# Kernel optimization log

Measured on AMD Instinct MI355X. Metric: run time of the kernel, lower is better.

The kernel has to match this reference:

```python
import jax, jax.numpy as jnp
import numpy as np

MODEL_DIM = 1024
NUM_HEADS = 16
DIM_PER_HEAD = MODEL_DIM // NUM_HEADS
LN_EPS = 1e-5


def setup_inputs() -> dict:
    key = jax.random.key(0)
    ks = jax.random.split(key, 5)
    B, S, D = 2, 2048, MODEL_DIM
    scale = 1.0 / np.sqrt(D)
    x = jax.random.normal(ks[0], (B, S, D), dtype=jnp.float32)
    # nn.Linear(bias=False) weights stored as [out, in]; we apply x @ W.T
    w_q = jax.random.normal(ks[1], (D, D), dtype=jnp.float32) * scale
    w_k = jax.random.normal(ks[2], (D, D), dtype=jnp.float32) * scale
    w_v = jax.random.normal(ks[3], (D, D), dtype=jnp.float32) * scale
    w_o = jax.random.normal(ks[4], (D, D), dtype=jnp.float32) * scale
    ln_gamma = jnp.ones((D,), dtype=jnp.float32)
    ln_beta = jnp.zeros((D,), dtype=jnp.float32)
    return {"x": x, "w_q": w_q, "w_k": w_k, "w_v": w_v, "w_o": w_o,
            "ln_gamma": ln_gamma, "ln_beta": ln_beta}


def _layer_norm(x, gamma, beta):
    mu = jnp.mean(x, axis=-1, keepdims=True)
    var = jnp.var(x, axis=-1, keepdims=True)
    return (x - mu) * jax.lax.rsqrt(var + LN_EPS) * gamma + beta


def reference(x, w_q, w_k, w_v, w_o, ln_gamma, ln_beta):
    B, S, D = x.shape
    H, Dh = NUM_HEADS, DIM_PER_HEAD
    residual = x
    # projections (Linear bias=False): x @ W.T
    q = (x @ w_q.T).reshape(B, S, H, Dh).transpose(0, 2, 1, 3)  # [B,H,S,Dh]
    k = (x @ w_k.T).reshape(B, S, H, Dh).transpose(0, 2, 1, 3)
    v = (x @ w_v.T).reshape(B, S, H, Dh).transpose(0, 2, 1, 3)
    scale = Dh ** (-0.5)
    scores = jnp.einsum('bhqd,bhkd->bhqk', q, k) * scale  # [B,H,Sq,Sk]
    # FAITHFUL quirk: nn.Softmax(dim=2) normalizes over the QUERY axis (axis=2)
    attn = jax.nn.softmax(scores, axis=2)
    # dropout is identity in eval mode
    ctx = jnp.einsum('bhqk,bhkd->bhqd', attn, v)  # [B,H,S,Dh]
    ctx = ctx.transpose(0, 2, 1, 3).reshape(B, S, D)
    out = ctx @ w_o.T
    return _layer_norm(residual + out, ln_gamma, ln_beta)
```

## Files before the change

### kernel.cpp

```cpp
#include <hip/hip_runtime.h>
#include <hip/hip_bf16.h>

constexpr int kB   = 2;
constexpr int kS   = 2048;
constexpr int kD   = 1024;
constexpr int kH   = 16;
constexpr int kDh  = 64;
constexpr int kBS  = kB * kS;

typedef __attribute__((ext_vector_type(8))) short short8;
typedef __attribute__((ext_vector_type(4))) float floatx4;
typedef __attribute__((ext_vector_type(16))) float floatx16;

__device__ inline unsigned short f2b(float f) {
    __hip_bfloat16 h = __float2bfloat16(f);
    return *reinterpret_cast<unsigned short*>(&h);
}

__device__ inline float b2f(unsigned short u) {
    union { unsigned u; float f; } cv;
    cv.u = (unsigned)u << 16;
    return cv.f;
}

__device__ inline floatx4 mfma16(short8 a, short8 b, floatx4 c) {
    return __builtin_amdgcn_mfma_f32_16x16x32_bf16(a, b, c, 0, 0, 0);
}

__device__ inline floatx16 mfma32(short8 a, short8 b, floatx16 c) {
    return __builtin_amdgcn_mfma_f32_32x32x16_bf16(a, b, c, 0, 0, 0);
}

__device__ inline unsigned packbf(float a, float b) {
    union { float f; unsigned u; } x, y;
    x.f = a; y.f = b;
    return (x.u >> 16) | (y.u & 0xffff0000u);
}

__device__ inline void gload16(const unsigned short* g, unsigned short* l) {
    __builtin_amdgcn_global_load_lds(
        (const __attribute__((address_space(1))) void*)g,
        (__attribute__((address_space(3))) void*)l, 16, 0, 0);
}

__global__ void convert_kernel(const float* __restrict__ x,
                               const float* __restrict__ wq, const float* __restrict__ wk,
                               const float* __restrict__ wv, const float* __restrict__ wo,
                               unsigned short* __restrict__ xb, unsigned short* __restrict__ wb) {
#pragma unroll
    for (int it = 0; it < 4; it++) {
        int gid = blockIdx.x * blockDim.x + threadIdx.x + it * (2048 * 256);
        long i4 = (long)gid * 4;
        const float* src;
        unsigned short* dst;
        long off;
        if (i4 < (long)kBS * kD) {
            src = x; dst = xb; off = i4;
        } else {
            long w = i4 - (long)kBS * kD;
            int sel = (int)(w >> 20);
            off = w & 1048575;
            src = (sel == 0) ? wq : (sel == 1) ? wk : (sel == 2) ? wv : wo;
            dst = wb + (long)sel * 1048576;
        }
        float4 v = *(const float4*)(src + off);
        ushort4 o;
        o.x = f2b(v.x); o.y = f2b(v.y); o.z = f2b(v.z); o.w = f2b(v.w);
        *(ushort4*)(dst + off) = o;
    }
}

template <int MODE>
__launch_bounds__(256, 3)
__global__ void gemm_nt(const unsigned short* __restrict__ A,
                        const unsigned short* __restrict__ Bw,
                        void* __restrict__ Cout,
                        const float* __restrict__ resid,
                        int M, int N, int K) {
    __shared__ __align__(16) unsigned short As[128 * 64];
    __shared__ __align__(16) unsigned short Bs[128 * 64];

    const int z  = blockIdx.z;
    const unsigned short* Bp = Bw + (size_t)z * N * K;
    const int m0 = blockIdx.y * 128, n0 = blockIdx.x * 128;
    const int tid  = threadIdx.x;
    const int lane = tid & 63, wv = tid >> 6;
    const int wm = wv >> 1, wn = wv & 1;
    const int quad = lane >> 4, l16 = lane & 15;

    floatx4 acc[4][4] = {};

    const int r0 = lane >> 3;
    const int jc = ((lane & 7) ^ r0) * 8;
    const unsigned short* Ag[4];
    const unsigned short* Bg[4];
    unsigned short* Asd[4];
    unsigned short* Bsd[4];
#pragma unroll
    for (int seg = 0; seg < 4; seg++) {
        const int row = seg * 32 + wv * 8 + r0;
        Ag[seg] = A  + (size_t)(m0 + row) * K + jc;
        Bg[seg] = Bp + (size_t)(n0 + row) * K + jc;
        Asd[seg] = As + (seg * 32 + wv * 8) * 64;
        Bsd[seg] = Bs + (seg * 32 + wv * 8) * 64;
    }

    const int pk0 = (quad ^ (l16 & 7)) * 8;
    const int pk1 = ((4 + quad) ^ (l16 & 7)) * 8;

    for (int k0 = 0; k0 < K; k0 += 64) {
        __syncthreads();
#pragma unroll
        for (int seg = 0; seg < 4; seg++) {
            gload16(Ag[seg] + k0, Asd[seg]);
            gload16(Bg[seg] + k0, Bsd[seg]);
        }
        __syncthreads();

#pragma unroll
        for (int h = 0; h < 2; h++) {
            const int pk = h ? pk1 : pk0;
            short8 af[4], bf[4];
#pragma unroll
            for (int i = 0; i < 4; i++)
                af[i] = *(const short8*)(As + (wm * 64 + i * 16 + l16) * 64 + pk);
#pragma unroll
            for (int j = 0; j < 4; j++)
                bf[j] = *(const short8*)(Bs + (wn * 64 + j * 16 + l16) * 64 + pk);
#pragma unroll
            for (int i = 0; i < 4; i++)
#pragma unroll
                for (int j = 0; j < 4; j++)
                    acc[i][j] = mfma16(af[i], bf[j], acc[i][j]);
        }
    }

#pragma unroll
    for (int i = 0; i < 4; i++)
#pragma unroll
        for (int j = 0; j < 4; j++) {
            const int row = m0 + wm * 64 + i * 16 + quad * 4;
            const int col = n0 + wn * 64 + j * 16 + l16;
#pragma unroll
            for (int r = 0; r < 4; r++) {
                float v = acc[i][j][r];
                if (MODE == 0) {
                    if (z == 0) v *= 0.18033688f;
                    ((unsigned short*)Cout)[(size_t)z * M * N + (size_t)(row + r) * N + col] = f2b(v);
                } else {
                    size_t idx = (size_t)(row + r) * N + col;
                    ((float*)Cout)[idx] = v + resid[idx];
                }
            }
        }
}

__launch_bounds__(256, 3)
__global__ void gemm_nt1(const unsigned short* __restrict__ A,
                         const unsigned short* __restrict__ Bw,
                         float* __restrict__ Cout,
                         const float* __restrict__ resid,
                         int M, int N, int K) {
    __shared__ __align__(16) unsigned short As[64 * 64];
    __shared__ __align__(16) unsigned short Bs[128 * 64];

    const int m0 = blockIdx.y * 64, n0 = blockIdx.x * 128;
    const int tid  = threadIdx.x;
    const int lane = tid & 63, wv = tid >> 6;
    const int wm = wv >> 1, wn = wv & 1;
    const int quad = lane >> 4, l16 = lane & 15;

    floatx4 acc[2][4] = {};

    const int r0 = lane >> 3;
    const int jc = ((lane & 7) ^ r0) * 8;
    const unsigned short* Ag[2];
    const unsigned short* Bg[4];
    unsigned short* Asd[2];
    unsigned short* Bsd[4];
#pragma unroll
    for (int seg = 0; seg < 2; seg++) {
        const int row = seg * 32 + wv * 8 + r0;
        Ag[seg]  = A + (size_t)(m0 + row) * K + jc;
        Asd[seg] = As + (seg * 32 + wv * 8) * 64;
    }
#pragma unroll
    for (int seg = 0; seg < 4; seg++) {
        const int row = seg * 32 + wv * 8 + r0;
        Bg[seg]  = Bw + (size_t)(n0 + row) * K + jc;
        Bsd[seg] = Bs + (seg * 32 + wv * 8) * 64;
    }

    const int pk0 = (quad ^ (l16 & 7)) * 8;
    const int pk1 = ((4 + quad) ^ (l16 & 7)) * 8;

    for (int k0 = 0; k0 < K; k0 += 64) {
        __syncthreads();
#pragma unroll
        for (int seg = 0; seg < 2; seg++)
            gload16(Ag[seg] + k0, Asd[seg]);
#pragma unroll
        for (int seg = 0; seg < 4; seg++)
            gload16(Bg[seg] + k0, Bsd[seg]);
        __syncthreads();

#pragma unroll
        for (int h = 0; h < 2; h++) {
            const int pk = h ? pk1 : pk0;
            short8 af[2], bf[4];
#pragma unroll
            for (int i = 0; i < 2; i++)
                af[i] = *(const short8*)(As + (wm * 32 + i * 16 + l16) * 64 + pk);
#pragma unroll
            for (int j = 0; j < 4; j++)
                bf[j] = *(const short8*)(Bs + (wn * 64 + j * 16 + l16) * 64 + pk);
#pragma unroll
            for (int i = 0; i < 2; i++)
#pragma unroll
                for (int j = 0; j < 4; j++)
                    acc[i][j] = mfma16(af[i], bf[j], acc[i][j]);
        }
    }

#pragma unroll
    for (int i = 0; i < 2; i++)
#pragma unroll
        for (int j = 0; j < 4; j++) {
            const int row = m0 + wm * 32 + i * 16 + quad * 4;
            const int col = n0 + wn * 64 + j * 16 + l16;
#pragma unroll
            for (int r = 0; r < 4; r++) {
                size_t idx = (size_t)(row + r) * N + col;
                Cout[idx] = acc[i][j][r] + resid[idx];
            }
        }
}

__launch_bounds__(256, 4)
__global__ void stats_vt_kernel(const unsigned short* __restrict__ Qb,
                                const unsigned short* __restrict__ Kb,
                                const unsigned short* __restrict__ Vb,
                                unsigned short* __restrict__ VT) {
    __shared__ __align__(16) unsigned short Qs[2][64 * 66];
    __shared__ float s_inv[64];

    const int id = blockIdx.x;
    const int bh = (id & 7) + 8 * ((id >> 3) & 3);
    const int keyblk = id >> 5;
    const int b = bh >> 4, h = bh & 15;
    const int tid = threadIdx.x, lane = tid & 63, w = tid >> 6;
    const int quad = lane >> 4, l16 = lane & 15;
    const int keybase = keyblk * 64 + w * 16;

    short8 ak0, ak1;
    {
        const unsigned short* Krow = Kb + (size_t)(b * kS + keybase + l16) * kD + h * kDh;
        ak0 = *(const short8*)(Krow + quad * 8);
        ak1 = *(const short8*)(Krow + 32 + quad * 8);
    }

    const int r0 = lane >> 3;
    const int jc = ((lane & 7) ^ r0) * 8;
    const unsigned short* Qg[2];
    int loff[2];
#pragma unroll
    for (int seg = 0; seg < 2; seg++) {
        const int row = w * 16 + seg * 8 + r0;
        Qg[seg] = Qb + (size_t)(b * kS + row) * kD + h * kDh + jc;
        loff[seg] = (w * 16 + seg * 8) * 64;
    }

    const int pk0 = (quad ^ (l16 & 7)) * 8;
    const int pk1 = ((4 + quad) ^ (l16 & 7)) * 8;

    float lacc[4] = {};

    for (int q0 = 0; q0 < kS; q0 += 128) {
        __syncthreads();
#pragma unroll
        for (int seg = 0; seg < 2; seg++) {
            gload16(Qg[seg] + (size_t)q0 * kD,        &Qs[0][loff[seg]]);
            gload16(Qg[seg] + (size_t)(q0 + 64) * kD, &Qs[1][loff[seg]]);
        }
        __syncthreads();

#pragma unroll
        for (int tb = 0; tb < 2; tb++) {
#pragma unroll
            for (int c = 0; c < 4; c++) {
                const unsigned short* row = &Qs[tb][(c * 16 + l16) * 64];
                short8 bq0 = *(const short8*)(row + pk0);
                short8 bq1 = *(const short8*)(row + pk1);
                floatx4 t = {0.f, 0.f, 0.f, 0.f};
                t = mfma16(ak0, bq0, t);
                t = mfma16(ak1, bq1, t);
#pragma unroll
                for (int r = 0; r < 4; r++)
                    lacc[r] += exp2f(t[r]);
            }
        }
    }

#pragma unroll
    for (int off = 1; off <= 8; off <<= 1)
#pragma unroll
        for (int r = 0; r < 4; r++)
            lacc[r] += __shfl_xor(lacc[r], off, 64);

    __syncthreads();
    if (l16 == 0) {
#pragma unroll
        for (int r = 0; r < 4; r++)
            s_inv[w * 16 + quad * 4 + r] = 1.0f / lacc[r];
    }
    __syncthreads();

    unsigned short* tile = &Qs[0][0];
    {
        const int kr = tid >> 2, dc = (tid & 3) * 16;
        const float iv = s_inv[kr];
        const unsigned short* src =
            Vb + (size_t)(b * kS + keyblk * 64 + kr) * kD + h * kDh + dc;
        unsigned short vs[16];
        *(uint4*)(vs)     = *(const uint4*)(src);
        *(uint4*)(vs + 8) = *(const uint4*)(src + 8);
#pragma unroll
        for (int i = 0; i < 16; i++)
            tile[kr * 65 + dc + i] = f2b(b2f(vs[i]) * iv);
    }
    __syncthreads();
    {
        const int d = tid >> 2, kc = (tid & 3) * 16;
        unsigned short os[16];
#pragma unroll
        for (int j = 0; j < 16; j++) os[j] = tile[(kc + j) * 65 + d];
        unsigned short* dst =
            VT + (size_t)bh * kDh * kS + (size_t)d * kS + keyblk * 64 + kc;
        *(uint4*)(dst)     = *(uint4*)(os);
        *(uint4*)(dst + 8) = *(uint4*)(os + 8);
    }
}

__launch_bounds__(256, 2)
__global__ void ctx_kernel(const unsigned short* __restrict__ Qb,
                           const unsigned short* __restrict__ Kb,
                           const unsigned short* __restrict__ VT,
                           unsigned short* __restrict__ Ctx) {
    __shared__ __align__(16) unsigned short Sh[2][2][64 * 64];

    const int id = blockIdx.x;
    const int bh = (id & 7) + 8 * ((id >> 3) & 3);
    const int qblk = id >> 5;
    const int b = bh >> 4, h = bh & 15;
    const int tid = threadIdx.x, lane = tid & 63, w = tid >> 6;
    const int l32 = lane & 31, hi = lane >> 5;
    const int qbase = qblk * 128 + w * 32;

    short8 aq[4];
    {
        const unsigned short* Qrow =
            Qb + (size_t)(b * kS + qbase + l32) * kD + h * kDh + hi * 8;
#pragma unroll
        for (int kq = 0; kq < 4; kq++)
            aq[kq] = *(const short8*)(Qrow + kq * 16);
    }
    floatx16 acc[2] = {};

    const unsigned short* Kbase = Kb + (size_t)(b * kS) * kD + h * kDh;
    const unsigned short* VTb   = VT + (size_t)bh * kDh * kS;

    const int r0 = lane >> 3;
    const int jc = ((lane & 7) ^ r0) * 8;
    const unsigned short* Kg[2];
    const unsigned short* Vg[2];
    int loff[2];
#pragma unroll
    for (int seg = 0; seg < 2; seg++) {
        const int row = w * 16 + seg * 8 + r0;
        Kg[seg] = Kbase + (size_t)row * kD + jc;
        Vg[seg] = VTb + (size_t)row * kS + jc;
        loff[seg] = (w * 16 + seg * 8) * 64;
    }

    const int x7 = l32 & 7;

    for (int k0 = 0; k0 < kS; k0 += 128) {
#pragma unroll
        for (int seg = 0; seg < 2; seg++) {
            gload16(Kg[seg] + (size_t)k0 * kD,        &Sh[0][0][loff[seg]]);
            gload16(Vg[seg] + k0,                     &Sh[0][1][loff[seg]]);
            gload16(Kg[seg] + (size_t)(k0 + 64) * kD, &Sh[1][0][loff[seg]]);
            gload16(Vg[seg] + (k0 + 64),              &Sh[1][1][loff[seg]]);
        }
        __syncthreads();

#pragma unroll
        for (int tb = 0; tb < 2; tb++) {
            const unsigned short* Ks  = Sh[tb][0];
            const unsigned short* VTs = Sh[tb][1];

            floatx16 sc[2];
#pragma unroll
            for (int s = 0; s < 2; s++) {
                const unsigned short* arow = Ks + (s * 32 + l32) * 64;
                floatx16 t = {0.f,0.f,0.f,0.f,0.f,0.f,0.f,0.f,
                              0.f,0.f,0.f,0.f,0.f,0.f,0.f,0.f};
#pragma unroll
                for (int kq = 0; kq < 4; kq++) {
                    short8 af = *(const short8*)(arow + ((2 * kq + hi) ^ x7) * 8);
                    t = mfma32(af, aq[kq], t);
                }
                sc[s] = t;
            }

            short8 pa[4];
#pragma unroll
            for (int s = 0; s < 2; s++) {
                float e[16];
#pragma unroll
                for (int r = 0; r < 16; r++) e[r] = exp2f(sc[s][r]);
                unsigned p0 = packbf(e[0],  e[1]),  p1 = packbf(e[2],  e[3]);
                unsigned p2 = packbf(e[4],  e[5]),  p3 = packbf(e[6],  e[7]);
                unsigned p4 = packbf(e[8],  e[9]),  p5 = packbf(e[10], e[11]);
                unsigned p6 = packbf(e[12], e[13]), p7 = packbf(e[14], e[15]);
                asm volatile("v_permlane32_swap_b32 %0, %1" : "+v"(p0), "+v"(p2));
                asm volatile("v_permlane32_swap_b32 %0, %1" : "+v"(p1), "+v"(p3));
                asm volatile("v_permlane32_swap_b32 %0, %1" : "+v"(p4), "+v"(p6));
                asm volatile("v_permlane32_swap_b32 %0, %1" : "+v"(p5), "+v"(p7));
                union { unsigned u[4]; short8 v; } f0, f1;
                f0.u[0] = p0; f0.u[1] = p1; f0.u[2] = p2; f0.u[3] = p3;
                f1.u[0] = p4; f1.u[1] = p5; f1.u[2] = p6; f1.u[3] = p7;
                pa[2 * s]     = f0.v;
                pa[2 * s + 1] = f1.v;
            }

#pragma unroll
            for (int t = 0; t < 2; t++) {
                const unsigned short* brow = VTs + (t * 32 + l32) * 64;
#pragma unroll
                for (int kk = 0; kk < 4; kk++) {
                    short8 bv = *(const short8*)(brow + ((2 * kk + hi) ^ x7) * 8);
                    acc[t] = mfma32(pa[kk], bv, acc[t]);
                }
            }
        }

        __syncthreads();
    }

#pragma unroll
    for (int t = 0; t < 2; t++)
#pragma unroll
        for (int rg = 0; rg < 4; rg++)
#pragma unroll
            for (int j = 0; j < 4; j++) {
                const int q = qbase + rg * 8 + hi * 4 + j;
                const int d = h * kDh + t * 32 + l32;
                Ctx[(size_t)(b * kS + q) * kD + d] = f2b(acc[t][rg * 4 + j]);
            }
}

__global__ void ln_kernel(const float* __restrict__ R, const float* __restrict__ gamma,
                          const float* __restrict__ beta, float* __restrict__ out) {
    const int tid = threadIdx.x, lane = tid & 63, w = tid >> 6;
    const int row = blockIdx.x * 4 + w;
    const float* Rr = R + (size_t)row * kD;
    float4 v[4];
    float s = 0.f, ss = 0.f;
#pragma unroll
    for (int c = 0; c < 4; c++) {
        v[c] = ((const float4*)Rr)[lane + 64 * c];
        s  += v[c].x + v[c].y + v[c].z + v[c].w;
        ss += v[c].x * v[c].x + v[c].y * v[c].y + v[c].z * v[c].z + v[c].w * v[c].w;
    }
#pragma unroll
    for (int off = 32; off > 0; off >>= 1) {
        s  += __shfl_down(s, off, 64);
        ss += __shfl_down(ss, off, 64);
    }
    const float S1 = __shfl(s, 0, 64);
    const float S2 = __shfl(ss, 0, 64);
    const float mu  = S1 * (1.0f / kD);
    const float inv = rsqrtf(S2 * (1.0f / kD) - mu * mu + 1e-5f);
    float* Or = out + (size_t)row * kD;
#pragma unroll
    for (int c = 0; c < 4; c++) {
        const float4 g  = ((const float4*)gamma)[lane + 64 * c];
        const float4 bb = ((const float4*)beta)[lane + 64 * c];
        float4 o;
        o.x = (v[c].x - mu) * inv * g.x + bb.x;
        o.y = (v[c].y - mu) * inv * g.y + bb.y;
        o.z = (v[c].z - mu) * inv * g.z + bb.z;
        o.w = (v[c].w - mu) * inv * g.w + bb.w;
        ((float4*)Or)[lane + 64 * c] = o;
    }
}

extern "C" void kernel_launch(void* const* d_in, const int* in_sizes, int n_in,
                              void* d_out, int out_size, void* d_ws, size_t ws_size,
                              hipStream_t stream) {
    const float* x     = (const float*)d_in[0];
    const float* wq    = (const float*)d_in[1];
    const float* wk    = (const float*)d_in[2];
    const float* wv    = (const float*)d_in[3];
    const float* wo    = (const float*)d_in[4];
    const float* gamma = (const float*)d_in[5];
    const float* beta  = (const float*)d_in[6];
    float* out = (float*)d_out;

    char* ws = (char*)d_ws;
    unsigned short* Xb  = (unsigned short*)(ws);
    unsigned short* Wb  = (unsigned short*)(ws + (8u  << 20));
    unsigned short* QKV = (unsigned short*)(ws + (16u << 20));
    unsigned short* Qb  = QKV;
    unsigned short* Kb  = QKV + (size_t)kBS * kD;
    unsigned short* Vb  = QKV + (size_t)2 * kBS * kD;
    unsigned short* Ctx = (unsigned short*)(ws + (40u << 20));
    unsigned short* VT  = (unsigned short*)(ws + (48u << 20));
    float* R            = (float*)(ws + (48u << 20));

    convert_kernel<<<2048, 256, 0, stream>>>(x, wq, wk, wv, wo, Xb, Wb);

    gemm_nt<0><<<dim3(kD / 128, kBS / 128, 3), 256, 0, stream>>>(
        Xb, Wb, QKV, nullptr, kBS, kD, kD);

    stats_vt_kernel<<<1024, 256, 0, stream>>>(Qb, Kb, Vb, VT);

    ctx_kernel<<<512, 256, 0, stream>>>(Qb, Kb, VT, Ctx);

    gemm_nt1<<<dim3(kD / 128, kBS / 64, 1), 256, 0, stream>>>(
        Ctx, Wb + (size_t)3 * kD * kD, R, x, kBS, kD, kD);

    ln_kernel<<<kBS / 4, 256, 0, stream>>>(R, gamma, beta, out);
}
```

Baseline: 235.5 us.

## Double-buffer GEMM shared-memory tiles with BK=32 to overlap loads and MFMA

Reworks the projection GEMM main loop to use two shared-memory buffers with a K-step of 32. The next tile is prefetched while MFMAs run on the current one, and the XOR swizzle is adjusted to the narrower row. This is meant to hide global-to-LDS latency and drop one of the two barriers per iteration. In exchange there are twice as many loop iterations and less MFMA work per barrier.

Result: no change. 236.9 us (+0.6%).

```diff
diff --git a/kernel.cpp b/kernel.cpp
--- a/kernel.cpp
+++ b/kernel.cpp
@@ -77,8 +77,7 @@
                         void* __restrict__ Cout,
                         const float* __restrict__ resid,
                         int M, int N, int K) {
-    __shared__ __align__(16) unsigned short As[128 * 64];
-    __shared__ __align__(16) unsigned short Bs[128 * 64];
+    __shared__ __align__(16) unsigned short Sh[2][2][128 * 32];
 
     const int z  = blockIdx.z;
     const unsigned short* Bp = Bw + (size_t)z * N * K;
@@ -90,49 +89,54 @@
 
     floatx4 acc[4][4] = {};
 
-    const int r0 = lane >> 3;
-    const int jc = ((lane & 7) ^ r0) * 8;
-    const unsigned short* Ag[4];
-    const unsigned short* Bg[4];
-    unsigned short* Asd[4];
-    unsigned short* Bsd[4];
-#pragma unroll
-    for (int seg = 0; seg < 4; seg++) {
-        const int row = seg * 32 + wv * 8 + r0;
-        Ag[seg] = A  + (size_t)(m0 + row) * K + jc;
-        Bg[seg] = Bp + (size_t)(n0 + row) * K + jc;
-        Asd[seg] = As + (seg * 32 + wv * 8) * 64;
-        Bsd[seg] = Bs + (seg * 32 + wv * 8) * 64;
-    }
-
-    const int pk0 = (quad ^ (l16 & 7)) * 8;
-    const int pk1 = ((4 + quad) ^ (l16 & 7)) * 8;
-
-    for (int k0 = 0; k0 < K; k0 += 64) {
-        __syncthreads();
-#pragma unroll
-        for (int seg = 0; seg < 4; seg++) {
-            gload16(Ag[seg] + k0, Asd[seg]);
-            gload16(Bg[seg] + k0, Bsd[seg]);
-        }
-        __syncthreads();
-
-#pragma unroll
-        for (int h = 0; h < 2; h++) {
-            const int pk = h ? pk1 : pk0;
-            short8 af[4], bf[4];
-#pragma unroll
-            for (int i = 0; i < 4; i++)
-                af[i] = *(const short8*)(As + (wm * 64 + i * 16 + l16) * 64 + pk);
+    const int lrow   = lane >> 2;
+    const int lchunk = (lane & 3) ^ (lrow & 3);
+    const unsigned short* Ag[2];
+    const unsigned short* Bg[2];
+    int loff[2];
+#pragma unroll
+    for (int seg = 0; seg < 2; seg++) {
+        const int g   = 2 * wv + seg;
+        const int row = 16 * g + lrow;
+        Ag[seg] = A  + (size_t)(m0 + row) * K + lchunk * 8;
+        Bg[seg] = Bp + (size_t)(n0 + row) * K + lchunk * 8;
+        loff[seg] = 16 * g * 32;
+    }
+
+    const int pk = (quad ^ (l16 & 3)) * 8;
+
+#pragma unroll
+    for (int seg = 0; seg < 2; seg++) {
+        gload16(Ag[seg], &Sh[0][0][loff[seg]]);
+        gload16(Bg[seg], &Sh[0][1][loff[seg]]);
+    }
+    __syncthreads();
+
+    int cur = 0;
+    for (int k0 = 0; k0 < K; k0 += 32) {
+        if (k0 + 32 < K) {
+#pragma unroll
+            for (int seg = 0; seg < 2; seg++) {
+                gload16(Ag[seg] + k0 + 32, &Sh[cur ^ 1][0][loff[seg]]);
+                gload16(Bg[seg] + k0 + 32, &Sh[cur ^ 1][1][loff[seg]]);
+            }
+        }
+        const unsigned short* As = Sh[cur][0];
+        const unsigned short* Bs = Sh[cur][1];
+        short8 af[4], bf[4];
+#pragma unroll
+        for (int i = 0; i < 4; i++)
+            af[i] = *(const short8*)(As + (wm * 64 + i * 16 + l16) * 32 + pk);
+#pragma unroll
+        for (int j = 0; j < 4; j++)
+            bf[j] = *(const short8*)(Bs + (wn * 64 + j * 16 + l16) * 32 + pk);
+#pragma unroll
+        for (int i = 0; i < 4; i++)
 #pragma unroll
             for (int j = 0; j < 4; j++)
-                bf[j] = *(const short8*)(Bs + (wn * 64 + j * 16 + l16) * 64 + pk);
-#pragma unroll
-            for (int i = 0; i < 4; i++)
-#pragma unroll
-                for (int j = 0; j < 4; j++)
-                    acc[i][j] = mfma16(af[i], bf[j], acc[i][j]);
-        }
+                acc[i][j] = mfma16(af[i], bf[j], acc[i][j]);
+        __syncthreads();
+        cur ^= 1;
     }
 
 #pragma unroll
```
